# Optimization experiments

Measured on AMD Instinct MI355X. Metric: run time of the kernel, lower is better.

## Reference

```python
import jax, jax.numpy as jnp
import numpy as np
from jax import lax

H = 1024        # lstm_hidden_size
V = 512         # action_vocab_size
WV = 300        # word_vec_size
S = 64          # step_num
N = 512         # entity_num


def setup_inputs() -> dict:
    key = jax.random.key(0)
    ks = jax.random.split(key, 16)
    s = 0.02
    return {
        "video_vectors": jax.random.normal(ks[0], (1, S, H), jnp.float32),
        "entity_vectors": jax.random.normal(ks[1], (N, H), jnp.float32),
        # action_selector: Linear(H,H) -> ReLU -> Dropout(eval: identity) -> Linear(H,V) -> Sigmoid
        "A1w": jax.random.normal(ks[2], (H, H), jnp.float32) * s,
        "A1b": jnp.zeros((H,), jnp.float32),
        "A2w": jax.random.normal(ks[3], (V, H), jnp.float32) * s,
        "A2b": jnp.zeros((V,), jnp.float32),
        "action_emb": jax.random.normal(ks[4], (V, WV), jnp.float32) * s,
        "W1w": jax.random.normal(ks[5], (H, H), jnp.float32) * s,
        "W1b": jnp.zeros((H,), jnp.float32),
        "W2w": jax.random.normal(ks[6], (H, H + V), jnp.float32) * s,
        "W2b": jnp.zeros((H,), jnp.float32),
        "W3w": jax.random.normal(ks[7], (3, H), jnp.float32) * s,
        "W3b": jnp.zeros((3,), jnp.float32),
        "W4w": jax.random.normal(ks[8], (1, WV), jnp.float32) * s,
        "W4b": jnp.zeros((1,), jnp.float32),
    }


def _forward(video_vectors, entity_vectors, A1w, A1b, A2w, A2b, action_emb,
             W1w, W1b, W2w, W2b, W3w, W3b, W4w, W4b):
    vv = video_vectors[0]                       # [S, H]
    n = entity_vectors.shape[0]

    def step(carry, v_ac):
        ev, prev_ent_attn = carry               # ev: [N, H], prev: [N]
        # action selector (dropout is identity in eval)
        h = jax.nn.relu(v_ac @ A1w.T + A1b)
        ac_prob = jax.nn.sigmoid(h @ A2w.T + A2b)        # [V]
        bar_ft = (ac_prob / ac_prob.sum()) @ action_emb  # [WV]
        hat_ht = jax.nn.relu(v_ac @ W1w.T + W1b)         # [H]
        w2v = jnp.concatenate([hat_ht, ac_prob]) @ W2w.T + W2b  # [H]
        ent_prob = jax.nn.sigmoid(ev @ w2v)              # [N]
        choice = jax.nn.softmax(hat_ht @ W3w.T + W3b)    # [3]
        attn = choice[0] * ent_prob + choice[1] * prev_ent_attn  # (choice[2]*0)
        bar_et = (attn / attn.sum()) @ ev                # [H]
        scal = bar_ft @ W4w[0] + W4b[0]                  # scalar (W4(bar_ft))
        kt = jax.nn.relu(scal * bar_et)                  # [H]
        ev_new = attn[:, None] * kt[None, :] + (1.0 - attn)[:, None] * ev  # [N, H]
        return (ev_new, ent_prob), (ent_prob, ac_prob, bar_et, ev_new, bar_ft)

    init = (entity_vectors, jnp.zeros((n,), entity_vectors.dtype))
    _, (ent_probs, ac_probs, step_ent, step_all, step_act) = lax.scan(step, init, vv)
    return ent_probs, ac_probs, step_ent, step_all, step_act


def reference(video_vectors, entity_vectors, A1w, A1b, A2w, A2b, action_emb,
              W1w, W1b, W2w, W2b, W3w, W3b, W4w, W4b):
    return _forward(video_vectors, entity_vectors, A1w, A1b, A2w, A2b, action_emb,
                    W1w, W1b, W2w, W2b, W3w, W3b, W4w, W4b)
```

## Files before the change

kernel.cpp:

```cpp
#include <hip/hip_runtime.h>

#define H  1024
#define V  512
#define WV 300
#define S  64
#define N  512

#define WS_HALL   0
#define WS_CAT    (S*H)
#define WS_W2V    (WS_CAT + S*1536)
#define WS_CHOICE (WS_W2V + S*H)
#define WS_SCAL   (WS_CHOICE + 2*S)
#define WS_ACSUM  (WS_SCAL + S)
#define WS_KT     (WS_ACSUM + S)
#define WS_ATT    (WS_KT + S*H)
#define WS_ACCUM  (WS_ATT + S*N)
#define WS_ASUM   (WS_ACCUM + 3*H)
#define WS_CTR    (WS_ASUM + 4)

#define OUT_EP   0
#define OUT_AC   (S*N)
#define OUT_SE   (S*N + S*V)
#define OUT_ALL  (OUT_SE + S*H)
#define OUT_ACT  (OUT_ALL + (size_t)S*N*H)

__device__ __forceinline__ float dot4(float4 a, float4 b) {
  return a.x*b.x + a.y*b.y + a.z*b.z + a.w*b.w;
}

struct GArgs {
  const float* X; const float* W0; const float* W1;
  const float* B0; const float* B1;
  float* o1_0; float* o1_1; float* o2_0; float* o2_1;
  int ldx, K, act, ld1_0, ld1_1, ld2_0, ld2_1;
};

#define KC 64
__global__ __launch_bounds__(256) void gemmNT(GArgs a) {
  __shared__ float Xs[64][KC + 4];
  __shared__ float Ws[64][KC + 4];
  const int tid = threadIdx.x;
  const int m = blockIdx.y;
  const float* W    = m ? a.W1 : a.W0;
  const float* bias = m ? a.B1 : a.B0;
  float* out1 = m ? a.o1_1 : a.o1_0;
  float* out2 = m ? a.o2_1 : a.o2_0;
  const int ld1 = m ? a.ld1_1 : a.ld1_0;
  const int ld2 = m ? a.ld2_1 : a.ld2_0;
  const int K = a.K;

  const int tm = tid >> 5, tn = tid & 31;
  const int jbase = blockIdx.x * 64;
  float acc[8][2];
#pragma unroll
  for (int i = 0; i < 8; ++i) acc[i][0] = acc[i][1] = 0.f;
  const int lr = tid >> 2;
  const int lc = (tid & 3) * 16;
  const float* xrow = a.X + (size_t)lr * a.ldx + lc;
  const float* wrow = W + (size_t)(jbase + lr) * K + lc;
  float4 xv0, xv1, xv2, xv3, wv0, wv1, wv2, wv3;
  xv0 = ((const float4*)xrow)[0]; xv1 = ((const float4*)xrow)[1];
  xv2 = ((const float4*)xrow)[2]; xv3 = ((const float4*)xrow)[3];
  wv0 = ((const float4*)wrow)[0]; wv1 = ((const float4*)wrow)[1];
  wv2 = ((const float4*)wrow)[2]; wv3 = ((const float4*)wrow)[3];
  for (int k0 = 0; k0 < K; k0 += KC) {
    __syncthreads();
    *(float4*)&Xs[lr][lc +  0] = xv0; *(float4*)&Xs[lr][lc +  4] = xv1;
    *(float4*)&Xs[lr][lc +  8] = xv2; *(float4*)&Xs[lr][lc + 12] = xv3;
    *(float4*)&Ws[lr][lc +  0] = wv0; *(float4*)&Ws[lr][lc +  4] = wv1;
    *(float4*)&Ws[lr][lc +  8] = wv2; *(float4*)&Ws[lr][lc + 12] = wv3;
    __syncthreads();
    if (k0 + KC < K) {
      const float* xp = xrow + k0 + KC;
      const float* wp = wrow + k0 + KC;
      xv0 = ((const float4*)xp)[0]; xv1 = ((const float4*)xp)[1];
      xv2 = ((const float4*)xp)[2]; xv3 = ((const float4*)xp)[3];
      wv0 = ((const float4*)wp)[0]; wv1 = ((const float4*)wp)[1];
      wv2 = ((const float4*)wp)[2]; wv3 = ((const float4*)wp)[3];
    }
#pragma unroll
    for (int kk = 0; kk < KC; kk += 4) {
      float4 w0 = *(const float4*)&Ws[tn][kk];
      float4 w1 = *(const float4*)&Ws[tn + 32][kk];
#pragma unroll
      for (int i = 0; i < 8; ++i) {
        float4 x = *(const float4*)&Xs[tm * 8 + i][kk];
        acc[i][0] += dot4(x, w0);
        acc[i][1] += dot4(x, w1);
      }
    }
  }
  const int j0 = jbase + tn, j1 = jbase + tn + 32;
  const float b0 = bias[j0], b1 = bias[j1];
#pragma unroll
  for (int i = 0; i < 8; ++i) {
    const int r = tm * 8 + i;
    float v0 = acc[i][0] + b0;
    float v1 = acc[i][1] + b1;
    if (a.act == 1) { v0 = fmaxf(v0, 0.f); v1 = fmaxf(v1, 0.f); }
    else if (a.act == 2) {
      v0 = 1.f / (1.f + __expf(-v0));
      v1 = 1.f / (1.f + __expf(-v1));
    }
    out1[(size_t)r * ld1 + j0] = v0;
    out1[(size_t)r * ld1 + j1] = v1;
    if (out2) {
      out2[(size_t)r * ld2 + j0] = v0;
      out2[(size_t)r * ld2 + j1] = v1;
    }
  }
}

__global__ void k_choice(const float* __restrict__ cat, const float* __restrict__ out_ac,
                         const float* __restrict__ W3w, const float* __restrict__ W3b,
                         float* __restrict__ ws) {
  int t = blockIdx.x, tid = threadIdx.x;
  const float* hat = cat + (size_t)t * 1536;
  float4 h4 = *(const float4*)(hat + tid * 4);
  float p[4];
#pragma unroll
  for (int r = 0; r < 3; ++r) {
    float4 w4 = *(const float4*)(W3w + (size_t)r * H + tid * 4);
    p[r] = dot4(h4, w4);
  }
  const float* ac = out_ac + (size_t)t * V;
  p[3] = ac[tid * 2] + ac[tid * 2 + 1];
  __shared__ float red[4][256];
#pragma unroll
  for (int q = 0; q < 4; ++q) red[q][tid] = p[q];
  __syncthreads();
  for (int sft = 128; sft > 0; sft >>= 1) {
    if (tid < sft) {
#pragma unroll
      for (int q = 0; q < 4; ++q) red[q][tid] += red[q][tid + sft];
    }
    __syncthreads();
  }
  if (tid == 0) {
    float l0 = red[0][0] + W3b[0], l1 = red[1][0] + W3b[1], l2 = red[2][0] + W3b[2];
    float m  = fmaxf(l0, fmaxf(l1, l2));
    float e0 = __expf(l0 - m), e1 = __expf(l1 - m), e2 = __expf(l2 - m);
    float inv = 1.f / (e0 + e1 + e2);
    ws[WS_CHOICE + t * 2]     = e0 * inv;
    ws[WS_CHOICE + t * 2 + 1] = e1 * inv;
    ws[WS_ACSUM + t]          = red[3][0];
  }
}

__global__ __launch_bounds__(256) void k_barft(
    const float* __restrict__ out_ac, const float* __restrict__ emb,
    const float* __restrict__ ws_ro, const float* __restrict__ W4w,
    const float* __restrict__ W4b, float* __restrict__ out_act,
    float* __restrict__ ws) {
  int t = blockIdx.x, tid = threadIdx.x;
  __shared__ float acS[V];
  const float* ac = out_ac + (size_t)t * V;
  acS[tid] = ac[tid];
  acS[tid + 256] = ac[tid + 256];
  __syncthreads();
  float s0 = 0.f, s1 = 0.f;
  const int w0 = tid, w1 = 256 + tid;
  for (int v = 0; v < V; ++v) {
    float a = acS[v];
    const float* er = emb + (size_t)v * WV;
    s0 += a * er[w0];
    if (tid < WV - 256) s1 += a * er[w1];
  }
  float inv = 1.f / ws_ro[WS_ACSUM + t];
  s0 *= inv; s1 *= inv;
  out_act[(size_t)t * WV + w0] = s0;
  if (tid < WV - 256) out_act[(size_t)t * WV + w1] = s1;
  float p = s0 * W4w[w0] + (tid < WV - 256 ? s1 * W4w[w1] : 0.f);
  __shared__ float red[256];
  red[tid] = p;
  __syncthreads();
  for (int s = 128; s > 0; s >>= 1) {
    if (tid < s) red[tid] += red[tid + s];
    __syncthreads();
  }
  if (tid == 0) ws[WS_SCAL + t] = red[0] + W4b[0];
}

__global__ __launch_bounds__(256) void k_seq(
    const float* __restrict__ ev0, const float* __restrict__ ws,
    float* __restrict__ accum, float* __restrict__ asum, unsigned* __restrict__ ctr,
    float* __restrict__ att, float* __restrict__ ktb,
    float* __restrict__ out_ep, float* __restrict__ out_se) {
  const int g = blockIdx.x, tid = threadIdx.x;
  const int lane = tid & 63, wv = tid >> 6;
  const int col = tid * 4;
  __shared__ float attnS[8], prevS[8], red[8][4];
  if (tid < 8) prevS[tid] = 0.f;
  float4 ev[8];
#pragma unroll
  for (int r = 0; r < 8; ++r)
    ev[r] = *(const float4*)(ev0 + (size_t)(g * 8 + r) * H + col);
  __syncthreads();
  unsigned target = 0;
  for (int t = 0; t < S; ++t) {
    const float4 w4 = *(const float4*)(ws + WS_W2V + (size_t)t * H + col);
    float dp[8];
#pragma unroll
    for (int r = 0; r < 8; ++r) dp[r] = dot4(ev[r], w4);
#pragma unroll
    for (int r = 0; r < 8; ++r) {
#pragma unroll
      for (int m = 32; m > 0; m >>= 1) dp[r] += __shfl_xor(dp[r], m, 64);
    }
    if (lane == 0) {
#pragma unroll
      for (int r = 0; r < 8; ++r) red[r][wv] = dp[r];
    }
    __syncthreads();
    if (tid < 8) {
      float d  = red[tid][0] + red[tid][1] + red[tid][2] + red[tid][3];
      float ep = 1.f / (1.f + __expf(-d));
      out_ep[(size_t)t * N + g * 8 + tid] = ep;
      float a = ws[WS_CHOICE + 2 * t] * ep + ws[WS_CHOICE + 2 * t + 1] * prevS[tid];
      prevS[tid] = ep;
      attnS[tid] = a;
      att[(size_t)t * N + g * 8 + tid] = a;
    }
    __syncthreads();
    float at[8];
#pragma unroll
    for (int r = 0; r < 8; ++r) at[r] = attnS[r];
    float4 pv = make_float4(0.f, 0.f, 0.f, 0.f);
#pragma unroll
    for (int r = 0; r < 8; ++r) {
      pv.x += at[r] * ev[r].x; pv.y += at[r] * ev[r].y;
      pv.z += at[r] * ev[r].z; pv.w += at[r] * ev[r].w;
    }
    float* acc = accum + (t % 3) * H;
    atomicAdd(acc + col + 0, pv.x);
    atomicAdd(acc + col + 1, pv.y);
    atomicAdd(acc + col + 2, pv.z);
    atomicAdd(acc + col + 3, pv.w);
    if (tid == 0) {
      float pa = 0.f;
#pragma unroll
      for (int r = 0; r < 8; ++r) pa += at[r];
      atomicAdd(asum + (t % 3), pa);
    }
    __syncthreads();
    target += (unsigned)gridDim.x;
    if (tid == 0) {
      __hip_atomic_fetch_add(ctr, 1u, __ATOMIC_RELEASE, __HIP_MEMORY_SCOPE_AGENT);
      while (__hip_atomic_load(ctr, __ATOMIC_RELAXED, __HIP_MEMORY_SCOPE_AGENT) < target) {}
      (void)__hip_atomic_load(ctr, __ATOMIC_ACQUIRE, __HIP_MEMORY_SCOPE_AGENT);
    }
    __syncthreads();
    float asv = __hip_atomic_load(asum + (t % 3), __ATOMIC_RELAXED, __HIP_MEMORY_SCOPE_AGENT);
    float4 pvs;
    pvs.x = __hip_atomic_load(acc + col + 0, __ATOMIC_RELAXED, __HIP_MEMORY_SCOPE_AGENT);
    pvs.y = __hip_atomic_load(acc + col + 1, __ATOMIC_RELAXED, __HIP_MEMORY_SCOPE_AGENT);
    pvs.z = __hip_atomic_load(acc + col + 2, __ATOMIC_RELAXED, __HIP_MEMORY_SCOPE_AGENT);
    pvs.w = __hip_atomic_load(acc + col + 3, __ATOMIC_RELAXED, __HIP_MEMORY_SCOPE_AGENT);
    float inv = 1.f / asv;
    float4 bar = make_float4(pvs.x * inv, pvs.y * inv, pvs.z * inv, pvs.w * inv);
    float sc = ws[WS_SCAL + t];
    float4 kt = make_float4(fmaxf(sc * bar.x, 0.f), fmaxf(sc * bar.y, 0.f),
                            fmaxf(sc * bar.z, 0.f), fmaxf(sc * bar.w, 0.f));
    if (g == 0) {
      *(float4*)(out_se + (size_t)t * H + col) = bar;
      *(float4*)(ktb + (size_t)t * H + col) = kt;
    }
    if (tid < 16)
      __hip_atomic_store(accum + ((t + 2) % 3) * H + g * 16 + tid, 0.f,
                         __ATOMIC_RELAXED, __HIP_MEMORY_SCOPE_AGENT);
    if (g == 0 && tid == 16)
      __hip_atomic_store(asum + ((t + 2) % 3), 0.f, __ATOMIC_RELAXED, __HIP_MEMORY_SCOPE_AGENT);
#pragma unroll
    for (int r = 0; r < 8; ++r) {
      float a = at[r];
      ev[r].x = a * kt.x + (1.f - a) * ev[r].x;
      ev[r].y = a * kt.y + (1.f - a) * ev[r].y;
      ev[r].z = a * kt.z + (1.f - a) * ev[r].z;
      ev[r].w = a * kt.w + (1.f - a) * ev[r].w;
    }
  }
}

__global__ __launch_bounds__(256) void k_recon(
    const float* __restrict__ ev0, const float* __restrict__ att,
    const float* __restrict__ ktb, float* __restrict__ out_all) {
  const int n = blockIdx.x, tid = threadIdx.x;
  const int col = tid * 4;
  __shared__ float aS[S];
  if (tid < S) aS[tid] = att[(size_t)tid * N + n];
  float4 v = *(const float4*)(ev0 + (size_t)n * H + col);
  __syncthreads();
  for (int t = 0; t < S; ++t) {
    float a = aS[t];
    float4 k4 = *(const float4*)(ktb + (size_t)t * H + col);
    v.x = a * k4.x + (1.f - a) * v.x;
    v.y = a * k4.y + (1.f - a) * v.y;
    v.z = a * k4.z + (1.f - a) * v.z;
    v.w = a * k4.w + (1.f - a) * v.w;
    *(float4*)(out_all + ((size_t)t * N + n) * H + col) = v;
  }
}

extern "C" void kernel_launch(void* const* d_in, const int* in_sizes, int n_in,
                              void* d_out, int out_size, void* d_ws, size_t ws_size,
                              hipStream_t stream) {
  const float* vv  = (const float*)d_in[0];
  const float* ev0 = (const float*)d_in[1];
  const float* A1w = (const float*)d_in[2];
  const float* A1b = (const float*)d_in[3];
  const float* A2w = (const float*)d_in[4];
  const float* A2b = (const float*)d_in[5];
  const float* emb = (const float*)d_in[6];
  const float* W1w = (const float*)d_in[7];
  const float* W1b = (const float*)d_in[8];
  const float* W2w = (const float*)d_in[9];
  const float* W2b = (const float*)d_in[10];
  const float* W3w = (const float*)d_in[11];
  const float* W3b = (const float*)d_in[12];
  const float* W4w = (const float*)d_in[13];
  const float* W4b = (const float*)d_in[14];

  float* ws  = (float*)d_ws;
  float* out = (float*)d_out;
  float* out_ep  = out + OUT_EP;
  float* out_ac  = out + OUT_AC;
  float* out_se  = out + OUT_SE;
  float* out_all = out + OUT_ALL;
  float* out_act = out + OUT_ACT;
  float* cat = ws + WS_CAT;

  hipMemsetAsync(ws + WS_ACCUM, 0, (size_t)(3 * H + 5) * sizeof(float), stream);

  {
    GArgs a{};
    a.X = vv; a.ldx = H; a.K = H; a.act = 1;
    a.W0 = A1w; a.B0 = A1b; a.o1_0 = ws + WS_HALL; a.ld1_0 = H;   a.o2_0 = nullptr; a.ld2_0 = 0;
    a.W1 = W1w; a.B1 = W1b; a.o1_1 = cat;          a.ld1_1 = 1536; a.o2_1 = nullptr; a.ld2_1 = 0;
    gemmNT<<<dim3(16, 2), 256, 0, stream>>>(a);
  }
  {
    GArgs a{};
    a.X = ws + WS_HALL; a.ldx = H; a.K = H; a.act = 2;
    a.W0 = A2w; a.B0 = A2b; a.o1_0 = out_ac; a.ld1_0 = V; a.o2_0 = cat + H; a.ld2_0 = 1536;
    a.W1 = A2w; a.B1 = A2b; a.o1_1 = out_ac; a.ld1_1 = V; a.o2_1 = cat + H; a.ld2_1 = 1536;
    gemmNT<<<dim3(8, 1), 256, 0, stream>>>(a);
  }
  k_choice<<<S, 256, 0, stream>>>(cat, out_ac, W3w, W3b, ws);
  {
    GArgs a{};
    a.X = cat; a.ldx = 1536; a.K = 1536; a.act = 0;
    a.W0 = W2w; a.B0 = W2b; a.o1_0 = ws + WS_W2V; a.ld1_0 = H; a.o2_0 = nullptr; a.ld2_0 = 0;
    a.W1 = W2w; a.B1 = W2b; a.o1_1 = ws + WS_W2V; a.ld1_1 = H; a.o2_1 = nullptr; a.ld2_1 = 0;
    gemmNT<<<dim3(16, 1), 256, 0, stream>>>(a);
  }
  k_barft<<<S, 256, 0, stream>>>(out_ac, emb, ws, W4w, W4b, out_act, ws);
  k_seq<<<64, 256, 0, stream>>>(ev0, ws, ws + WS_ACCUM, ws + WS_ASUM,
                                (unsigned*)(ws + WS_CTR),
                                ws + WS_ATT, ws + WS_KT, out_ep, out_se);
  k_recon<<<N, 256, 0, stream>>>(ev0, ws + WS_ATT, ws + WS_KT, out_all);
}
```

Baseline: 1.267 ms.

## Split-K the small GEMMs and shrink the recurrent grid to eight blocks

The three projection GEMMs, which launched only 8-32 blocks, now use an 8-way split-K kernel that writes partial sums into scratch space borrowed from the out_all region. A separate epilogue kernel then reduces the partials and applies bias and the activation. The sequential recurrence kernel moves from 64 blocks of 256 threads to 8 blocks of 1024 threads. Each block writes its partial attention-weighted sums to double-buffered slots instead of making global atomicAdds into a zeroed triple buffer, which cuts grid-barrier participants and atomic contention per step. The cost is extra launches, an extra partial-sum round trip through memory, and each block reading all 8 slots after every barrier.

```diff
diff --git a/kernel.cpp b/kernel.cpp
--- a/kernel.cpp
+++ b/kernel.cpp
@@ -5,6 +5,9 @@
 #define WV 300
 #define S  64
 #define N  512
+
+#define KP 8
+#define KC 64
 
 #define WS_HALL   0
 #define WS_CAT    (S*H)
@@ -14,9 +17,9 @@
 #define WS_ACSUM  (WS_SCAL + S)
 #define WS_KT     (WS_ACSUM + S)
 #define WS_ATT    (WS_KT + S*H)
-#define WS_ACCUM  (WS_ATT + S*N)
-#define WS_ASUM   (WS_ACCUM + 3*H)
-#define WS_CTR    (WS_ASUM + 4)
+#define WS_SLOTP  (WS_ATT + S*N)
+#define WS_SLOTA  (WS_SLOTP + 2*8*1024)
+#define WS_CTR    (WS_SLOTA + 16)
 
 #define OUT_EP   0
 #define OUT_AC   (S*N)
@@ -28,49 +31,40 @@
   return a.x*b.x + a.y*b.y + a.z*b.z + a.w*b.w;
 }
 
-struct GArgs {
+struct SKArgs {
   const float* X; const float* W0; const float* W1;
-  const float* B0; const float* B1;
-  float* o1_0; float* o1_1; float* o2_0; float* o2_1;
-  int ldx, K, act, ld1_0, ld1_1, ld2_0, ld2_1;
+  float* pbuf;
+  int ldx, K, KS, Ntot;
 };
 
-#define KC 64
-__global__ __launch_bounds__(256) void gemmNT(GArgs a) {
+__global__ __launch_bounds__(256) void g_split(SKArgs a) {
   __shared__ float Xs[64][KC + 4];
   __shared__ float Ws[64][KC + 4];
   const int tid = threadIdx.x;
-  const int m = blockIdx.y;
-  const float* W    = m ? a.W1 : a.W0;
-  const float* bias = m ? a.B1 : a.B0;
-  float* out1 = m ? a.o1_1 : a.o1_0;
-  float* out2 = m ? a.o2_1 : a.o2_0;
-  const int ld1 = m ? a.ld1_1 : a.ld1_0;
-  const int ld2 = m ? a.ld2_1 : a.ld2_0;
-  const int K = a.K;
-
+  const int jt = blockIdx.x, kp = blockIdx.y, mat = blockIdx.z;
+  const float* W = mat ? a.W1 : a.W0;
+  const int jbase = jt * 64, kbase = kp * a.KS;
   const int tm = tid >> 5, tn = tid & 31;
-  const int jbase = blockIdx.x * 64;
   float acc[8][2];
 #pragma unroll
   for (int i = 0; i < 8; ++i) acc[i][0] = acc[i][1] = 0.f;
   const int lr = tid >> 2;
   const int lc = (tid & 3) * 16;
-  const float* xrow = a.X + (size_t)lr * a.ldx + lc;
-  const float* wrow = W + (size_t)(jbase + lr) * K + lc;
+  const float* xrow = a.X + (size_t)lr * a.ldx + kbase + lc;
+  const float* wrow = W + (size_t)(jbase + lr) * a.K + kbase + lc;
   float4 xv0, xv1, xv2, xv3, wv0, wv1, wv2, wv3;
   xv0 = ((const float4*)xrow)[0]; xv1 = ((const float4*)xrow)[1];
   xv2 = ((const float4*)xrow)[2]; xv3 = ((const float4*)xrow)[3];
   wv0 = ((const float4*)wrow)[0]; wv1 = ((const float4*)wrow)[1];
   wv2 = ((const float4*)wrow)[2]; wv3 = ((const float4*)wrow)[3];
-  for (int k0 = 0; k0 < K; k0 += KC) {
+  for (int k0 = 0; k0 < a.KS; k0 += KC) {
     __syncthreads();
     *(float4*)&Xs[lr][lc +  0] = xv0; *(float4*)&Xs[lr][lc +  4] = xv1;
     *(float4*)&Xs[lr][lc +  8] = xv2; *(float4*)&Xs[lr][lc + 12] = xv3;
     *(float4*)&Ws[lr][lc +  0] = wv0; *(float4*)&Ws[lr][lc +  4] = wv1;
     *(float4*)&Ws[lr][lc +  8] = wv2; *(float4*)&Ws[lr][lc + 12] = wv3;
     __syncthreads();
-    if (k0 + KC < K) {
+    if (k0 + KC < a.KS) {
       const float* xp = xrow + k0 + KC;
       const float* wp = wrow + k0 + KC;
       xv0 = ((const float4*)xp)[0]; xv1 = ((const float4*)xp)[1];
@@ -90,25 +84,40 @@
       }
     }
   }
-  const int j0 = jbase + tn, j1 = jbase + tn + 32;
-  const float b0 = bias[j0], b1 = bias[j1];
+  float* base = a.pbuf + ((size_t)(mat * KP + kp) * 64) * a.Ntot + jbase;
 #pragma unroll
   for (int i = 0; i < 8; ++i) {
     const int r = tm * 8 + i;
-    float v0 = acc[i][0] + b0;
-    float v1 = acc[i][1] + b1;
-    if (a.act == 1) { v0 = fmaxf(v0, 0.f); v1 = fmaxf(v1, 0.f); }
-    else if (a.act == 2) {
-      v0 = 1.f / (1.f + __expf(-v0));
-      v1 = 1.f / (1.f + __expf(-v1));
-    }
-    out1[(size_t)r * ld1 + j0] = v0;
-    out1[(size_t)r * ld1 + j1] = v1;
-    if (out2) {
-      out2[(size_t)r * ld2 + j0] = v0;
-      out2[(size_t)r * ld2 + j1] = v1;
-    }
-  }
+    base[(size_t)r * a.Ntot + tn]      = acc[i][0];
+    base[(size_t)r * a.Ntot + tn + 32] = acc[i][1];
+  }
+}
+
+struct EPArgs {
+  const float* pbuf;
+  const float* B0; const float* B1;
+  float* o1_0; float* o2_0; float* o1_1; float* o2_1;
+  int nsh, ld1_0, ld2_0, ld1_1, ld2_1, act;
+};
+
+__global__ __launch_bounds__(256) void ep_k(EPArgs e) {
+  const int mat = blockIdx.y;
+  const int Ntot = 1 << e.nsh;
+  const int idx = blockIdx.x * 256 + threadIdx.x;
+  const int r = idx >> e.nsh, j = idx & (Ntot - 1);
+  const float* pb = e.pbuf + (size_t)mat * KP * 64 * Ntot;
+  float s = 0.f;
+#pragma unroll
+  for (int kp = 0; kp < KP; ++kp) s += pb[(size_t)(kp * 64 + r) * Ntot + j];
+  s += (mat ? e.B1 : e.B0)[j];
+  if (e.act == 1) s = fmaxf(s, 0.f);
+  else if (e.act == 2) s = 1.f / (1.f + __expf(-s));
+  float* o1 = mat ? e.o1_1 : e.o1_0;
+  float* o2 = mat ? e.o2_1 : e.o2_0;
+  const int ld1 = mat ? e.ld1_1 : e.ld1_0;
+  const int ld2 = mat ? e.ld2_1 : e.ld2_0;
+  o1[(size_t)r * ld1 + j] = s;
+  if (o2) o2[(size_t)r * ld2 + j] = s;
 }
 
 __global__ void k_choice(const float* __restrict__ cat, const float* __restrict__ out_ac,
@@ -181,66 +190,80 @@
   if (tid == 0) ws[WS_SCAL + t] = red[0] + W4b[0];
 }
 
-__global__ __launch_bounds__(256) void k_seq(
+__global__ __launch_bounds__(1024, 1) void k_seq(
     const float* __restrict__ ev0, const float* __restrict__ ws,
-    float* __restrict__ accum, float* __restrict__ asum, unsigned* __restrict__ ctr,
+    float* __restrict__ slotP, float* __restrict__ slotA, unsigned* __restrict__ ctr,
     float* __restrict__ att, float* __restrict__ ktb,
     float* __restrict__ out_ep, float* __restrict__ out_se) {
   const int g = blockIdx.x, tid = threadIdx.x;
-  const int lane = tid & 63, wv = tid >> 6;
-  const int col = tid * 4;
-  __shared__ float attnS[8], prevS[8], red[8][4];
-  if (tid < 8) prevS[tid] = 0.f;
-  float4 ev[8];
-#pragma unroll
-  for (int r = 0; r < 8; ++r)
-    ev[r] = *(const float4*)(ev0 + (size_t)(g * 8 + r) * H + col);
+  const int c = tid & 255, rg = tid >> 8;
+  const int col = c * 4;
+  const int wave = tid >> 6, lane = tid & 63;
+  __shared__ float dpred[16][16];
+  __shared__ float attnS[64], prevS[64];
+  __shared__ alignas(16) float parts[3][256][4];
+  if (tid < 64) prevS[tid] = 0.f;
+  float4 ev[16];
+#pragma unroll
+  for (int i = 0; i < 16; ++i)
+    ev[i] = *(const float4*)(ev0 + (size_t)(g * 64 + rg * 16 + i) * H + col);
   __syncthreads();
   unsigned target = 0;
   for (int t = 0; t < S; ++t) {
+    const int buf = t & 1;
     const float4 w4 = *(const float4*)(ws + WS_W2V + (size_t)t * H + col);
-    float dp[8];
-#pragma unroll
-    for (int r = 0; r < 8; ++r) dp[r] = dot4(ev[r], w4);
-#pragma unroll
-    for (int r = 0; r < 8; ++r) {
-#pragma unroll
-      for (int m = 32; m > 0; m >>= 1) dp[r] += __shfl_xor(dp[r], m, 64);
+    float dp[16];
+#pragma unroll
+    for (int i = 0; i < 16; ++i) dp[i] = dot4(ev[i], w4);
+#pragma unroll
+    for (int m = 32; m > 0; m >>= 1) {
+#pragma unroll
+      for (int i = 0; i < 16; ++i) dp[i] += __shfl_xor(dp[i], m, 64);
     }
     if (lane == 0) {
 #pragma unroll
-      for (int r = 0; r < 8; ++r) red[r][wv] = dp[r];
-    }
-    __syncthreads();
-    if (tid < 8) {
-      float d  = red[tid][0] + red[tid][1] + red[tid][2] + red[tid][3];
+      for (int i = 0; i < 16; ++i) dpred[wave][i] = dp[i];
+    }
+    __syncthreads();
+    if (tid < 64) {
+      const int r = tid, rgr = r >> 4, ri = r & 15;
+      float d = dpred[rgr * 4][ri] + dpred[rgr * 4 + 1][ri]
+              + dpred[rgr * 4 + 2][ri] + dpred[rgr * 4 + 3][ri];
       float ep = 1.f / (1.f + __expf(-d));
-      out_ep[(size_t)t * N + g * 8 + tid] = ep;
-      float a = ws[WS_CHOICE + 2 * t] * ep + ws[WS_CHOICE + 2 * t + 1] * prevS[tid];
-      prevS[tid] = ep;
-      attnS[tid] = a;
-      att[(size_t)t * N + g * 8 + tid] = a;
-    }
-    __syncthreads();
-    float at[8];
-#pragma unroll
-    for (int r = 0; r < 8; ++r) at[r] = attnS[r];
+      out_ep[(size_t)t * N + g * 64 + r] = ep;
+      float a = ws[WS_CHOICE + 2 * t] * ep + ws[WS_CHOICE + 2 * t + 1] * prevS[r];
+      prevS[r] = ep;
+      attnS[r] = a;
+      att[(size_t)t * N + g * 64 + r] = a;
+      float s = a;
+#pragma unroll
+      for (int m = 32; m > 0; m >>= 1) s += __shfl_xor(s, m, 64);
+      if (tid == 0)
+        __hip_atomic_store(slotA + buf * 8 + g, s, __ATOMIC_RELAXED, __HIP_MEMORY_SCOPE_AGENT);
+    }
+    __syncthreads();
+    float atl[16];
+#pragma unroll
+    for (int i = 0; i < 16; ++i) atl[i] = attnS[rg * 16 + i];
     float4 pv = make_float4(0.f, 0.f, 0.f, 0.f);
 #pragma unroll
-    for (int r = 0; r < 8; ++r) {
-      pv.x += at[r] * ev[r].x; pv.y += at[r] * ev[r].y;
-      pv.z += at[r] * ev[r].z; pv.w += at[r] * ev[r].w;
-    }
-    float* acc = accum + (t % 3) * H;
-    atomicAdd(acc + col + 0, pv.x);
-    atomicAdd(acc + col + 1, pv.y);
-    atomicAdd(acc + col + 2, pv.z);
-    atomicAdd(acc + col + 3, pv.w);
-    if (tid == 0) {
-      float pa = 0.f;
-#pragma unroll
-      for (int r = 0; r < 8; ++r) pa += at[r];
-      atomicAdd(asum + (t % 3), pa);
+    for (int i = 0; i < 16; ++i) {
+      pv.x += atl[i] * ev[i].x; pv.y += atl[i] * ev[i].y;
+      pv.z += atl[i] * ev[i].z; pv.w += atl[i] * ev[i].w;
+    }
+    if (rg > 0) *(float4*)&parts[rg - 1][c][0] = pv;
+    __syncthreads();
+    if (rg == 0) {
+#pragma unroll
+      for (int j = 0; j < 3; ++j) {
+        float4 q = *(const float4*)&parts[j][c][0];
+        pv.x += q.x; pv.y += q.y; pv.z += q.z; pv.w += q.w;
+      }
+      float* sp = slotP + (size_t)(buf * 8 + g) * 1024 + col;
+      __hip_atomic_store(sp + 0, pv.x, __ATOMIC_RELAXED, __HIP_MEMORY_SCOPE_AGENT);
+      __hip_atomic_store(sp + 1, pv.y, __ATOMIC_RELAXED, __HIP_MEMORY_SCOPE_AGENT);
+      __hip_atomic_store(sp + 2, pv.z, __ATOMIC_RELAXED, __HIP_MEMORY_SCOPE_AGENT);
+      __hip_atomic_store(sp + 3, pv.w, __ATOMIC_RELAXED, __HIP_MEMORY_SCOPE_AGENT);
     }
     __syncthreads();
     target += (unsigned)gridDim.x;
@@ -250,33 +273,33 @@
       (void)__hip_atomic_load(ctr, __ATOMIC_ACQUIRE, __HIP_MEMORY_SCOPE_AGENT);
     }
     __syncthreads();
-    float asv = __hip_atomic_load(asum + (t % 3), __ATOMIC_RELAXED, __HIP_MEMORY_SCOPE_AGENT);
-    float4 pvs;
-    pvs.x = __hip_atomic_load(acc + col + 0, __ATOMIC_RELAXED, __HIP_MEMORY_SCOPE_AGENT);
-    pvs.y = __hip_atomic_load(acc + col + 1, __ATOMIC_RELAXED, __HIP_MEMORY_SCOPE_AGENT);
-    pvs.z = __hip_atomic_load(acc + col + 2, __ATOMIC_RELAXED, __HIP_MEMORY_SCOPE_AGENT);
-    pvs.w = __hip_atomic_load(acc + col + 3, __ATOMIC_RELAXED, __HIP_MEMORY_SCOPE_AGENT);
+    float4 bar = make_float4(0.f, 0.f, 0.f, 0.f);
+    float asv = 0.f;
+#pragma unroll
+    for (int b = 0; b < 8; ++b) {
+      const float* sp = slotP + (size_t)(buf * 8 + b) * 1024 + col;
+      bar.x += __hip_atomic_load(sp + 0, __ATOMIC_RELAXED, __HIP_MEMORY_SCOPE_AGENT);
+      bar.y += __hip_atomic_load(sp + 1, __ATOMIC_RELAXED, __HIP_MEMORY_SCOPE_AGENT);
+      bar.z += __hip_atomic_load(sp + 2, __ATOMIC_RELAXED, __HIP_MEMORY_SCOPE_AGENT);
+      bar.w += __hip_atomic_load(sp + 3, __ATOMIC_RELAXED, __HIP_MEMORY_SCOPE_AGENT);
+      asv   += __hip_atomic_load(slotA + buf * 8 + b, __ATOMIC_RELAXED, __HIP_MEMORY_SCOPE_AGENT);
+    }
     float inv = 1.f / asv;
-    float4 bar = make_float4(pvs.x * inv, pvs.y * inv, pvs.z * inv, pvs.w * inv);
+    bar.x *= inv; bar.y *= inv; bar.z *= inv; bar.w *= inv;
     float sc = ws[WS_SCAL + t];
     float4 kt = make_float4(fmaxf(sc * bar.x, 0.f), fmaxf(sc * bar.y, 0.f),
                             fmaxf(sc * bar.z, 0.f), fmaxf(sc * bar.w, 0.f));
-    if (g == 0) {
+    if (g == 0 && rg == 0) {
       *(float4*)(out_se + (size_t)t * H + col) = bar;
       *(float4*)(ktb + (size_t)t * H + col) = kt;
     }
-    if (tid < 16)
-      __hip_atomic_store(accum + ((t + 2) % 3) * H + g * 16 + tid, 0.f,
-                         __ATOMIC_RELAXED, __HIP_MEMORY_SCOPE_AGENT);
-    if (g == 0 && tid == 16)
-      __hip_atomic_store(asum + ((t + 2) % 3), 0.f, __ATOMIC_RELAXED, __HIP_MEMORY_SCOPE_AGENT);
-#pragma unroll
-    for (int r = 0; r < 8; ++r) {
-      float a = at[r];
-      ev[r].x = a * kt.x + (1.f - a) * ev[r].x;
-      ev[r].y = a * kt.y + (1.f - a) * ev[r].y;
-      ev[r].z = a * kt.z + (1.f - a) * ev[r].z;
-      ev[r].w = a * kt.w + (1.f - a) * ev[r].w;
+#pragma unroll
+    for (int i = 0; i < 16; ++i) {
+      float a = atl[i];
+      ev[i].x = a * kt.x + (1.f - a) * ev[i].x;
+      ev[i].y = a * kt.y + (1.f - a) * ev[i].y;
+      ev[i].z = a * kt.z + (1.f - a) * ev[i].z;
+      ev[i].w = a * kt.w + (1.f - a) * ev[i].w;
     }
   }
 }
@@ -328,33 +351,31 @@
   float* out_all = out + OUT_ALL;
   float* out_act = out + OUT_ACT;
   float* cat = ws + WS_CAT;
-
-  hipMemsetAsync(ws + WS_ACCUM, 0, (size_t)(3 * H + 5) * sizeof(float), stream);
+  float* P   = out_all;
+
+  hipMemsetAsync(ws + WS_CTR, 0, sizeof(unsigned), stream);
 
   {
-    GArgs a{};
-    a.X = vv; a.ldx = H; a.K = H; a.act = 1;
-    a.W0 = A1w; a.B0 = A1b; a.o1_0 = ws + WS_HALL; a.ld1_0 = H;   a.o2_0 = nullptr; a.ld2_0 = 0;
-    a.W1 = W1w; a.B1 = W1b; a.o1_1 = cat;          a.ld1_1 = 1536; a.o2_1 = nullptr; a.ld2_1 = 0;
-    gemmNT<<<dim3(16, 2), 256, 0, stream>>>(a);
+    SKArgs a{vv, A1w, W1w, P, H, H, H / KP, H};
+    g_split<<<dim3(16, KP, 2), 256, 0, stream>>>(a);
+    EPArgs e{P, A1b, W1b, ws + WS_HALL, nullptr, cat, nullptr, 10, H, 0, 1536, 0, 1};
+    ep_k<<<dim3(256, 2), 256, 0, stream>>>(e);
   }
   {
-    GArgs a{};
-    a.X = ws + WS_HALL; a.ldx = H; a.K = H; a.act = 2;
-    a.W0 = A2w; a.B0 = A2b; a.o1_0 = out_ac; a.ld1_0 = V; a.o2_0 = cat + H; a.ld2_0 = 1536;
-    a.W1 = A2w; a.B1 = A2b; a.o1_1 = out_ac; a.ld1_1 = V; a.o2_1 = cat + H; a.ld2_1 = 1536;
-    gemmNT<<<dim3(8, 1), 256, 0, stream>>>(a);
+    SKArgs a{ws + WS_HALL, A2w, A2w, P, H, H, H / KP, V};
+    g_split<<<dim3(8, KP, 1), 256, 0, stream>>>(a);
+    EPArgs e{P, A2b, A2b, out_ac, cat + H, nullptr, nullptr, 9, V, 1536, 0, 0, 2};
+    ep_k<<<dim3(128, 1), 256, 0, stream>>>(e);
   }
   k_choice<<<S, 256, 0, stream>>>(cat, out_ac, W3w, W3b, ws);
   {
-    GArgs a{};
-    a.X = cat; a.ldx = 1536; a.K = 1536; a.act = 0;
-    a.W0 = W2w; a.B0 = W2b; a.o1_0 = ws + WS_W2V; a.ld1_0 = H; a.o2_0 = nullptr; a.ld2_0 = 0;
-    a.W1 = W2w; a.B1 = W2b; a.o1_1 = ws + WS_W2V; a.ld1_1 = H; a.o2_1 = nullptr; a.ld2_1 = 0;
-    gemmNT<<<dim3(16, 1), 256, 0, stream>>>(a);
+    SKArgs a{cat, W2w, W2w, P, 1536, 1536, 1536 / KP, H};
+    g_split<<<dim3(16, KP, 1), 256, 0, stream>>>(a);
+    EPArgs e{P, W2b, W2b, ws + WS_W2V, nullptr, nullptr, nullptr, 10, H, 0, 0, 0, 0};
+    ep_k<<<dim3(256, 1), 256, 0, stream>>>(e);
   }
   k_barft<<<S, 256, 0, stream>>>(out_ac, emb, ws, W4w, W4b, out_act, ws);
-  k_seq<<<64, 256, 0, stream>>>(ev0, ws, ws + WS_ACCUM, ws + WS_ASUM,
+  k_seq<<<8, 1024, 0, stream>>>(ev0, ws, ws + WS_SLOTP, ws + WS_SLOTA,
                                 (unsigned*)(ws + WS_CTR),
                                 ws + WS_ATT, ws + WS_KT, out_ep, out_se);
   k_recon<<<N, 256, 0, stream>>>(ev0, ws + WS_ATT, ws + WS_KT, out_all);
```

Result: slower. 1.509 ms (+19.1%).
